# Performance work log

Hardware: AMD Instinct MI355X
Metric: run time of the kernel (lower is better)

## Reference

```python
import jax, jax.numpy as jnp
import numpy as np

B, LT, D, N, H = 16, 512, 1024, 4096, 16
LN_EPS = 1e-5


def setup_inputs() -> dict:
    key = jax.random.key(0)
    ks = jax.random.split(key, 10)
    s = 0.02
    struct_token = jax.random.normal(ks[0], (N, D), dtype=jnp.float32)
    text_token = jax.random.normal(ks[1], (B, LT, D), dtype=jnp.float32)
    # contiguous, sorted segment ids: 256 struct tokens per batch element
    struct_batch = jnp.repeat(jnp.arange(B, dtype=jnp.int32), N // B)
    return {
        "struct_token": struct_token,
        "text_token": text_token,
        "in_proj_w": jax.random.normal(ks[2], (3 * D, D), dtype=jnp.float32) * s,
        "in_proj_b": jnp.zeros((3 * D,), jnp.float32),
        "attn_out_w": jax.random.normal(ks[3], (D, D), dtype=jnp.float32) * s,
        "attn_out_b": jnp.zeros((D,), jnp.float32),
        "ln_g": jnp.ones((D,), jnp.float32),
        "ln_b": jnp.zeros((D,), jnp.float32),
        "proj_w": jax.random.normal(ks[4], (D, D), dtype=jnp.float32) * s,
        "proj_b": jnp.zeros((D,), jnp.float32),
        "struct_batch": struct_batch,
        "L_max": N // B,
    }


def reference(struct_token, text_token, in_proj_w, in_proj_b, attn_out_w,
              attn_out_b, ln_g, ln_b, proj_w, proj_b, struct_batch, L_max):
    Bq = text_token.shape[0]
    Dm = struct_token.shape[-1]
    dh = Dm // H
    Ntok = struct_token.shape[0]

    # ---- ragged pad-pack (struct_batch is sorted/contiguous per segment) ----
    counts = jnp.bincount(struct_batch, length=Bq)                 # [B]
    starts = jnp.concatenate([jnp.zeros((1,), counts.dtype),
                              jnp.cumsum(counts)[:-1]])            # [B]
    pos = jnp.arange(Ntok) - starts[struct_batch]                  # [N] position in segment
    padded = jnp.zeros((Bq, L_max, Dm), struct_token.dtype)
    padded = padded.at[struct_batch, pos].set(struct_token)        # [B, Ls, D]

    # ---- nn.MultiheadAttention (batch_first): Q=padded, K=V=text ----
    wq, wk, wv = in_proj_w[:Dm], in_proj_w[Dm:2 * Dm], in_proj_w[2 * Dm:]
    bq, bk, bv = in_proj_b[:Dm], in_proj_b[Dm:2 * Dm], in_proj_b[2 * Dm:]
    q = (padded @ wq.T + bq).reshape(Bq, L_max, H, dh)
    k = (text_token @ wk.T + bk).reshape(Bq, -1, H, dh)
    v = (text_token @ wv.T + bv).reshape(Bq, -1, H, dh)
    scores = jnp.einsum('bqhd,bkhd->bhqk', q, k) / jnp.sqrt(jnp.float32(dh))
    attn = jax.nn.softmax(scores, axis=-1)
    ctx = jnp.einsum('bhqk,bkhd->bqhd', attn, v).reshape(Bq, L_max, Dm)
    fused = ctx @ attn_out_w.T + attn_out_b                        # [B, Ls, D]

    # ---- LayerNorm + output projection ----
    mu = fused.mean(-1, keepdims=True)
    var = fused.var(-1, keepdims=True)
    fused = (fused - mu) * jax.lax.rsqrt(var + LN_EPS) * ln_g + ln_b
    fused = fused @ proj_w.T + proj_b

    # ---- unpack valid tokens + scatter-mean over segments ----
    tok = fused[struct_batch, pos]                                 # [N, D]
    seg_sum = jax.ops.segment_sum(tok, struct_batch, num_segments=Bq)
    return seg_sum / jnp.maximum(counts, 1)[:, None].astype(seg_sum.dtype)
```

## Files before the change

### kernel.cpp

```cpp
#include <hip/hip_runtime.h>

constexpr int B  = 16;
constexpr int LT = 512;
constexpr int D  = 1024;
constexpr int N  = 4096;
constexpr int H  = 16;
constexpr int DH = D / H;
constexpr int LMAX = N / B;
constexpr float LN_EPS = 1e-5f;

typedef short  s16x8 __attribute__((ext_vector_type(8)));
typedef float  f32x4 __attribute__((ext_vector_type(4)));

__device__ __forceinline__ unsigned short f2bf(float x) {
    unsigned int u = __float_as_uint(x);
    unsigned int r = (u + 0x7fffu + ((u >> 16) & 1u)) >> 16;
    return (unsigned short)r;
}
__device__ __forceinline__ float bf2f(unsigned short u) {
    return __uint_as_float((unsigned int)u << 16);
}

__device__ __forceinline__ void load_lds16(const void* g, void* l) {
    __builtin_amdgcn_global_load_lds(
        (const __attribute__((address_space(1))) unsigned int*)g,
        (__attribute__((address_space(3))) unsigned int*)l, 16, 0, 0);
}

__global__ void prep_kernel(const int* __restrict__ sb, int* __restrict__ counts,
                            int* __restrict__ starts, int* __restrict__ pos) {
    __shared__ int s_counts[B], s_starts[B];
    int t = threadIdx.x;
    if (t < B) s_counts[t] = 0;
    __syncthreads();
    for (int i = t; i < N; i += 256) atomicAdd(&s_counts[sb[i]], 1);
    __syncthreads();
    if (t == 0) {
        int run = 0;
        for (int b = 0; b < B; b++) { s_starts[b] = run; run += s_counts[b]; }
    }
    __syncthreads();
    if (t < B) { counts[t] = s_counts[t]; starts[t] = s_starts[t]; }
    for (int i = t; i < N; i += 256) {
        int b = sb[i];
        pos[i] = i - s_starts[b];
    }
}

__global__ void scatter_kernel(const float* __restrict__ st, const int* __restrict__ sb,
                               const int* __restrict__ pos, unsigned short* __restrict__ padded) {
    int i = blockIdx.x;
    int b = sb[i], p = pos[i];
    int d = threadIdx.x * 4;
    float4 v = *(const float4*)&st[(size_t)i * D + d];
    ushort4 o;
    o.x = f2bf(v.x); o.y = f2bf(v.y); o.z = f2bf(v.z); o.w = f2bf(v.w);
    *(ushort4*)&padded[((size_t)(b * LMAX + p)) * D + d] = o;
}

__global__ __launch_bounds__(256) void cast3_kernel(
        const float* __restrict__ x0, unsigned short* __restrict__ y0, int n0,
        const float* __restrict__ x1, unsigned short* __restrict__ y1, int n1,
        const float* __restrict__ x2, unsigned short* __restrict__ y2, int n2) {
    long long i = (long long)(blockIdx.x * 256 + threadIdx.x) * 8;
    const float* x; unsigned short* y;
    if (i < n0)                { x = x0 + i; y = y0 + i; }
    else if (i < (long long)n0 + n1) { long long j = i - n0; x = x1 + j; y = y1 + j; }
    else if (i < (long long)n0 + n1 + n2) { long long j = i - n0 - n1; x = x2 + j; y = y2 + j; }
    else return;
    float4 a = *(const float4*)x;
    float4 b = *(const float4*)(x + 4);
    ushort4 o1, o2;
    o1.x = f2bf(a.x); o1.y = f2bf(a.y); o1.z = f2bf(a.z); o1.w = f2bf(a.w);
    o2.x = f2bf(b.x); o2.y = f2bf(b.y); o2.z = f2bf(b.z); o2.w = f2bf(b.w);
    *(ushort4*)y = o1;
    *(ushort4*)(y + 4) = o2;
}

constexpr int PANEL = 128 * 32;

template<typename Epi>
__device__ __forceinline__ void gemm_tile_e(const unsigned short* __restrict__ A,
                                            const unsigned short* __restrict__ W,
                                            int K, int m0, int n0,
                                            unsigned short* As, unsigned short* Bs,
                                            Epi&& epi) {
    const int tid  = threadIdx.x;
    const int lane = tid & 63;
    const int wave = tid >> 6;
    const int wm = (wave >> 1) * 64, wn = (wave & 1) * 64;

    const int srow = tid >> 2;
    const int scol = (tid & 3) * 8;
    const unsigned short* Ag = A + (size_t)(m0 + srow) * K + scol;
    const unsigned short* Wg = W + (size_t)(n0 + srow) * K + scol;
    unsigned short* Asl = As + tid * 8;
    unsigned short* Bsl = Bs + tid * 8;

    const int fm = lane & 15;
    const int fk = (lane >> 4) * 8;

    f32x4 acc[4][4];
#pragma unroll
    for (int i = 0; i < 4; i++)
#pragma unroll
        for (int j = 0; j < 4; j++) acc[i][j] = (f32x4){0.f, 0.f, 0.f, 0.f};

    for (int k0 = 0; k0 < K; k0 += 64) {
        __syncthreads();
        load_lds16(Ag + k0, Asl);
        load_lds16(Ag + (size_t)64 * K + k0, Asl + 64 * 32);
        load_lds16(Wg + k0, Bsl);
        load_lds16(Wg + (size_t)64 * K + k0, Bsl + 64 * 32);
        load_lds16(Ag + k0 + 32, Asl + PANEL);
        load_lds16(Ag + (size_t)64 * K + k0 + 32, Asl + PANEL + 64 * 32);
        load_lds16(Wg + k0 + 32, Bsl + PANEL);
        load_lds16(Wg + (size_t)64 * K + k0 + 32, Bsl + PANEL + 64 * 32);
        __syncthreads();

#pragma unroll
        for (int hp = 0; hp < 2; hp++) {
            const unsigned short* Ap = As + hp * PANEL;
            const unsigned short* Bp = Bs + hp * PANEL;
            s16x8 af[4], bf[4];
#pragma unroll
            for (int i = 0; i < 4; i++) {
                af[i] = *(const s16x8*)&Ap[(wm + i * 16 + fm) * 32 + fk];
                bf[i] = *(const s16x8*)&Bp[(wn + i * 16 + fm) * 32 + fk];
            }
#pragma unroll
            for (int i = 0; i < 4; i++)
#pragma unroll
                for (int j = 0; j < 4; j++)
                    acc[i][j] = __builtin_amdgcn_mfma_f32_16x16x32_bf16(af[i], bf[j], acc[i][j], 0, 0, 0);
        }
    }

    const int fr = (lane >> 4) * 4;
#pragma unroll
    for (int j = 0; j < 4; j++) {
        int col = n0 + wn + j * 16 + fm;
#pragma unroll
        for (int i = 0; i < 4; i++) {
            int row = m0 + wm + i * 16 + fr;
#pragma unroll
            for (int r = 0; r < 4; r++)
                epi(row + r, col, acc[i][j][r]);
        }
    }
}

__global__ __launch_bounds__(256) void qkv_fused(const unsigned short* __restrict__ padded,
                                                 const unsigned short* __restrict__ text,
                                                 const unsigned short* __restrict__ wqkv,
                                                 const float* __restrict__ bqkv,
                                                 unsigned short* __restrict__ qpack,
                                                 unsigned short* __restrict__ kpack,
                                                 unsigned short* __restrict__ vpack) {
    __shared__ __align__(16) unsigned short As[2 * PANEL];
    __shared__ __align__(16) unsigned short Bs[2 * PANEL];
    int flat = blockIdx.x;
    if (flat < 256) {
        gemm_tile_e(padded, wqkv, D, (flat >> 3) * 128, (flat & 7) * 128, As, Bs,
            [&](int m, int col, float v) {
                float val = v + bqkv[col];
                int b = m >> 8, q = m & 255;
                int h = col >> 6, d = col & 63;
                qpack[(size_t)(b * H + h) * 16384 + (d >> 3) * 2048 + q * 8 + (d & 7)] = f2bf(val);
            });
    } else if (flat < 768) {
        int f = flat - 256;
        gemm_tile_e(text, wqkv + (size_t)D * D, D, (f >> 3) * 128, (f & 7) * 128, As, Bs,
            [&](int m, int col, float v) {
                float val = v + bqkv[D + col];
                int b = m >> 9, key = m & 511;
                int h = col >> 6, d = col & 63;
                kpack[(size_t)(b * H + h) * 32768 + (d >> 3) * 4096 + key * 8 + (d & 7)] = f2bf(val);
            });
    } else {
        int f = flat - 768;
        gemm_tile_e(wqkv + 2 * (size_t)D * D, text, D, (f >> 6) * 128, (f & 63) * 128, As, Bs,
            [&](int m, int col, float v) {
                float val = v + bqkv[2 * D + m];
                int h = m >> 6, d = m & 63;
                int b = col >> 9, key = col & 511;
                vpack[(size_t)(b * H + h) * 32768 + (key >> 3) * 512 + d * 8 + (key & 7)] = f2bf(val);
            });
    }
}

__global__ __launch_bounds__(256) void gemm_bf(const unsigned short* __restrict__ A,
                                               const unsigned short* __restrict__ W,
                                               const float* __restrict__ bias,
                                               unsigned short* __restrict__ C, int Nn, int K) {
    __shared__ __align__(16) unsigned short As[2 * PANEL];
    __shared__ __align__(16) unsigned short Bs[2 * PANEL];
    gemm_tile_e(A, W, K, blockIdx.y * 128, blockIdx.x * 128, As, Bs,
        [&](int m, int col, float v) {
            C[(size_t)m * Nn + col] = f2bf(v + bias[col]);
        });
}

constexpr int PKW = 72;

__global__ __launch_bounds__(512) void attn_mfma(const unsigned short* __restrict__ qpack,
                                                 const unsigned short* __restrict__ kpack,
                                                 const unsigned short* __restrict__ vpack,
                                                 unsigned short* __restrict__ ctx) {
    __shared__ __align__(16) unsigned short KV[16384];
    __shared__ __align__(16) unsigned short Ps[8 * 16 * PKW];

    const int tid = threadIdx.x;
    const int lane = tid & 63;
    const int wv = tid >> 6;
    const int fm = lane & 15;
    const int quad = lane >> 4;
    const int h = blockIdx.x, b = blockIdx.y, half = blockIdx.z;
    const int q0 = half * 128 + wv * 16;

    const unsigned short* qp = qpack + (size_t)(b * H + h) * 16384;
    const unsigned short* kp = kpack + (size_t)(b * H + h) * 32768;
    const unsigned short* vp = vpack + (size_t)(b * H + h) * 32768;

    const s16x8 aq0 = *(const s16x8*)&qp[quad * 2048 + (q0 + fm) * 8];
    const s16x8 aq1 = *(const s16x8*)&qp[(4 + quad) * 2048 + (q0 + fm) * 8];

    f32x4 sc[32];

    for (int kc = 0; kc < 2; kc++) {
        __syncthreads();
#pragma unroll
        for (int it = 0; it < 4; it++) {
            int f = it * 512 + tid;
            load_lds16(kp + (f >> 8) * 4096 + kc * 2048 + (f & 255) * 8, KV + f * 8);
        }
        __syncthreads();
#pragma unroll
        for (int t = 0; t < 16; t++) {
            s16x8 bk0 = *(const s16x8*)&KV[quad * 2048 + (t * 16 + fm) * 8];
            s16x8 bk1 = *(const s16x8*)&KV[(4 + quad) * 2048 + (t * 16 + fm) * 8];
            f32x4 a = (f32x4){0.f, 0.f, 0.f, 0.f};
            a = __builtin_amdgcn_mfma_f32_16x16x32_bf16(aq0, bk0, a, 0, 0, 0);
            a = __builtin_amdgcn_mfma_f32_16x16x32_bf16(aq1, bk1, a, 0, 0, 0);
            sc[kc * 16 + t] = a;
        }
    }

    const float scale = 0.125f;
    float mx[4], l[4], inv[4];
#pragma unroll
    for (int r = 0; r < 4; r++) {
        float m = sc[0][r];
#pragma unroll
        for (int t = 1; t < 32; t++) m = fmaxf(m, sc[t][r]);
        mx[r] = m;
    }
#pragma unroll
    for (int o = 1; o < 16; o <<= 1)
#pragma unroll
        for (int r = 0; r < 4; r++) mx[r] = fmaxf(mx[r], __shfl_xor(mx[r], o));
#pragma unroll
    for (int r = 0; r < 4; r++) l[r] = 0.f;
#pragma unroll
    for (int t = 0; t < 32; t++)
#pragma unroll
        for (int r = 0; r < 4; r++) {
            float e = __expf((sc[t][r] - mx[r]) * scale);
            sc[t][r] = e;
            l[r] += e;
        }
#pragma unroll
    for (int o = 1; o < 16; o <<= 1)
#pragma unroll
        for (int r = 0; r < 4; r++) l[r] += __shfl_xor(l[r], o);
#pragma unroll
    for (int r = 0; r < 4; r++) inv[r] = 1.f / l[r];

    f32x4 co[4];
#pragma unroll
    for (int n = 0; n < 4; n++) co[n] = (f32x4){0.f, 0.f, 0.f, 0.f};
    unsigned short* Pw = Ps + wv * (16 * PKW);

    for (int vc = 0; vc < 2; vc++) {
        __syncthreads();
#pragma unroll
        for (int it = 0; it < 4; it++) {
            int f = it * 512 + tid;
            load_lds16(vp + vc * 16384 + f * 8, KV + f * 8);
        }
        __syncthreads();
        for (int cs = 0; cs < 4; cs++) {
            int c = vc * 4 + cs;
#pragma unroll
            for (int tt = 0; tt < 4; tt++)
#pragma unroll
                for (int r = 0; r < 4; r++)
                    Pw[(quad * 4 + r) * PKW + tt * 16 + fm] = f2bf(sc[c * 4 + tt][r]);
#pragma unroll
            for (int s = 0; s < 2; s++) {
                s16x8 ap = *(const s16x8*)&Pw[fm * PKW + s * 32 + quad * 8];
#pragma unroll
                for (int n = 0; n < 4; n++) {
                    s16x8 bv = *(const s16x8*)&KV[(cs * 8 + s * 4 + quad) * 512 + (n * 16 + fm) * 8];
                    co[n] = __builtin_amdgcn_mfma_f32_16x16x32_bf16(ap, bv, co[n], 0, 0, 0);
                }
            }
        }
    }

    const size_t obase = (size_t)(b * LMAX + q0) * D + h * DH;
#pragma unroll
    for (int n = 0; n < 4; n++)
#pragma unroll
        for (int r = 0; r < 4; r++)
            ctx[obase + (size_t)(quad * 4 + r) * D + n * 16 + fm] = f2bf(co[n][r] * inv[r]);
}

__global__ __launch_bounds__(256) void lnmean_kernel(const unsigned short* __restrict__ f1,
                                                     const float* __restrict__ g,
                                                     const float* __restrict__ bb,
                                                     const int* __restrict__ counts,
                                                     float* __restrict__ msum) {
    int b = blockIdx.x;
    int cnt = counts[b];
    int s0 = blockIdx.y * 32;
    int s1 = min(cnt, s0 + 32);
    if (s0 >= s1) return;
    int t = threadIdx.x;
    int wv = t >> 6, ln = t & 63;
    float4 gg = ((const float4*)g)[t];
    float4 bv = ((const float4*)bb)[t];
    float acc[4] = {0.f, 0.f, 0.f, 0.f};
    __shared__ float red[8];

    for (int s = s0; s < s1; s++) {
        const unsigned short* x = f1 + ((size_t)(b * LMAX + s)) * D;
        ushort4 u = ((const ushort4*)x)[t];
        float4 val = {bf2f(u.x), bf2f(u.y), bf2f(u.z), bf2f(u.w)};
        float sm = val.x + val.y + val.z + val.w;
        float ss = val.x * val.x + val.y * val.y + val.z * val.z + val.w * val.w;
#pragma unroll
        for (int o = 32; o; o >>= 1) { sm += __shfl_xor(sm, o); ss += __shfl_xor(ss, o); }
        if (ln == 0) { red[wv] = sm; red[4 + wv] = ss; }
        __syncthreads();
        sm = red[0] + red[1] + red[2] + red[3];
        ss = red[4] + red[5] + red[6] + red[7];
        __syncthreads();
        float mu = sm * (1.f / D);
        float var = ss * (1.f / D) - mu * mu;
        float r = rsqrtf(var + LN_EPS);
        acc[0] += (val.x - mu) * r * gg.x + bv.x;
        acc[1] += (val.y - mu) * r * gg.y + bv.y;
        acc[2] += (val.z - mu) * r * gg.z + bv.z;
        acc[3] += (val.w - mu) * r * gg.w + bv.w;
    }
    float inv = 1.f / (float)max(cnt, 1);
#pragma unroll
    for (int j = 0; j < 4; j++)
        atomicAdd(&msum[(size_t)b * D + t * 4 + j], acc[j] * inv);
}

__global__ __launch_bounds__(256) void tproj_kernel(const float* __restrict__ msum,
                                                    const float* __restrict__ W,
                                                    const float* __restrict__ bias,
                                                    float* __restrict__ out) {
    int lane = threadIdx.x & 63;
    int n = blockIdx.x * 4 + (threadIdx.x >> 6);
    float4 wr[4];
#pragma unroll
    for (int i = 0; i < 4; i++)
        wr[i] = *(const float4*)&W[(size_t)n * D + i * 256 + lane * 4];
    float bn = bias[n];
    for (int b = 0; b < B; b++) {
        float s = 0.f;
#pragma unroll
        for (int i = 0; i < 4; i++) {
            float4 m4 = *(const float4*)&msum[(size_t)b * D + i * 256 + lane * 4];
            s += m4.x * wr[i].x + m4.y * wr[i].y + m4.z * wr[i].z + m4.w * wr[i].w;
        }
#pragma unroll
        for (int o = 32; o; o >>= 1) s += __shfl_xor(s, o);
        if (lane == 0) out[(size_t)b * D + n] = s + bn;
    }
}

extern "C" void kernel_launch(void* const* d_in, const int* in_sizes, int n_in,
                              void* d_out, int out_size, void* d_ws, size_t ws_size,
                              hipStream_t stream) {
    const float* struct_token = (const float*)d_in[0];
    const float* text_token   = (const float*)d_in[1];
    const float* in_proj_w    = (const float*)d_in[2];
    const float* in_proj_b    = (const float*)d_in[3];
    const float* attn_out_w   = (const float*)d_in[4];
    const float* attn_out_b   = (const float*)d_in[5];
    const float* ln_g         = (const float*)d_in[6];
    const float* ln_b         = (const float*)d_in[7];
    const float* proj_w       = (const float*)d_in[8];
    const float* proj_b       = (const float*)d_in[9];
    const int*   sb           = (const int*)d_in[10];
    float* out = (float*)d_out;

    const size_t MQ  = (size_t)B * LMAX;
    const size_t MKV = (size_t)B * LT;

    char* p = (char*)d_ws;
    unsigned short* padded_b = (unsigned short*)p;  p += MQ * D * 2;
    unsigned short* text_b   = (unsigned short*)p;  p += MKV * D * 2;
    unsigned short* wqkv_b   = (unsigned short*)p;  p += (size_t)3 * D * D * 2;
    unsigned short* wattn_b  = (unsigned short*)p;  p += (size_t)D * D * 2;
    unsigned short* qpack    = (unsigned short*)p;  p += MQ * D * 2;
    unsigned short* kpack    = (unsigned short*)p;  p += MKV * D * 2;
    unsigned short* vpack    = (unsigned short*)p;  p += MKV * D * 2;
    unsigned short* ctx_b    = (unsigned short*)p;  p += MQ * D * 2;
    unsigned short* f1b      = (unsigned short*)p;  p += MQ * D * 2;
    float* msum = (float*)p;  p += (size_t)B * D * 4;
    int* pos    = (int*)p;  p += N * 4;
    int* counts = (int*)p;  p += B * 4;
    int* starts = (int*)p;  p += B * 4;

    hipMemsetAsync(padded_b, 0, MQ * D * 2, stream);
    hipMemsetAsync(msum, 0, (size_t)B * D * 4, stream);
    prep_kernel<<<1, 256, 0, stream>>>(sb, counts, starts, pos);
    scatter_kernel<<<N, 256, 0, stream>>>(struct_token, sb, pos, padded_b);

    cast3_kernel<<<6144, 256, 0, stream>>>(
        text_token, text_b, (int)(MKV * D),
        in_proj_w,  wqkv_b, 3 * D * D,
        attn_out_w, wattn_b, D * D);

    qkv_fused<<<1280, 256, 0, stream>>>(padded_b, text_b, wqkv_b, in_proj_b,
                                        qpack, kpack, vpack);

    attn_mfma<<<dim3(H, B, 2), 512, 0, stream>>>(qpack, kpack, vpack, ctx_b);

    gemm_bf<<<dim3(D / 128, MQ / 128), 256, 0, stream>>>(ctx_b, wattn_b, attn_out_b, f1b, D, D);

    lnmean_kernel<<<dim3(B, LMAX / 32), 256, 0, stream>>>(f1b, ln_g, ln_b, counts, msum);

    tproj_kernel<<<256, 256, 0, stream>>>(msum, proj_w, proj_b, out);
}
```

Before: 286.7 us.

## Fold segment prep into cast kernel, drop memset and pos, per-wave LayerNorm rows

```diff
diff --git a/kernel.cpp b/kernel.cpp
--- a/kernel.cpp
+++ b/kernel.cpp
@@ -27,42 +27,26 @@
         (__attribute__((address_space(3))) unsigned int*)l, 16, 0, 0);
 }
 
-__global__ void prep_kernel(const int* __restrict__ sb, int* __restrict__ counts,
-                            int* __restrict__ starts, int* __restrict__ pos) {
-    __shared__ int s_counts[B], s_starts[B];
-    int t = threadIdx.x;
-    if (t < B) s_counts[t] = 0;
-    __syncthreads();
-    for (int i = t; i < N; i += 256) atomicAdd(&s_counts[sb[i]], 1);
-    __syncthreads();
-    if (t == 0) {
-        int run = 0;
-        for (int b = 0; b < B; b++) { s_starts[b] = run; run += s_counts[b]; }
-    }
-    __syncthreads();
-    if (t < B) { counts[t] = s_counts[t]; starts[t] = s_starts[t]; }
-    for (int i = t; i < N; i += 256) {
-        int b = sb[i];
-        pos[i] = i - s_starts[b];
-    }
-}
-
-__global__ void scatter_kernel(const float* __restrict__ st, const int* __restrict__ sb,
-                               const int* __restrict__ pos, unsigned short* __restrict__ padded) {
-    int i = blockIdx.x;
-    int b = sb[i], p = pos[i];
-    int d = threadIdx.x * 4;
-    float4 v = *(const float4*)&st[(size_t)i * D + d];
-    ushort4 o;
-    o.x = f2bf(v.x); o.y = f2bf(v.y); o.z = f2bf(v.z); o.w = f2bf(v.w);
-    *(ushort4*)&padded[((size_t)(b * LMAX + p)) * D + d] = o;
-}
-
-__global__ __launch_bounds__(256) void cast3_kernel(
+__global__ __launch_bounds__(256) void cast3_prep(
         const float* __restrict__ x0, unsigned short* __restrict__ y0, int n0,
         const float* __restrict__ x1, unsigned short* __restrict__ y1, int n1,
-        const float* __restrict__ x2, unsigned short* __restrict__ y2, int n2) {
-    long long i = (long long)(blockIdx.x * 256 + threadIdx.x) * 8;
+        const float* __restrict__ x2, unsigned short* __restrict__ y2, int n2,
+        const int* __restrict__ sb, int* __restrict__ counts, int* __restrict__ starts) {
+    __shared__ int s_counts[B];
+    int t = threadIdx.x;
+    if (blockIdx.x == 6144) {
+        if (t < B) s_counts[t] = 0;
+        __syncthreads();
+        for (int i = t; i < N; i += 256) atomicAdd(&s_counts[sb[i]], 1);
+        __syncthreads();
+        if (t == 0) {
+            int run = 0;
+            for (int b = 0; b < B; b++) { starts[b] = run; run += s_counts[b]; }
+        }
+        if (t < B) counts[t] = s_counts[t];
+        return;
+    }
+    long long i = (long long)(blockIdx.x * 256 + t) * 8;
     const float* x; unsigned short* y;
     if (i < n0)                { x = x0 + i; y = y0 + i; }
     else if (i < (long long)n0 + n1) { long long j = i - n0; x = x1 + j; y = y1 + j; }
@@ -75,6 +59,21 @@
     o2.x = f2bf(b.x); o2.y = f2bf(b.y); o2.z = f2bf(b.z); o2.w = f2bf(b.w);
     *(ushort4*)y = o1;
     *(ushort4*)(y + 4) = o2;
+}
+
+__global__ void scatter_full(const float* __restrict__ st,
+                             const int* __restrict__ counts,
+                             const int* __restrict__ starts,
+                             unsigned short* __restrict__ padded) {
+    int p = blockIdx.x, b = blockIdx.y;
+    int d = threadIdx.x * 4;
+    size_t off = ((size_t)(b * LMAX + p)) * D + d;
+    ushort4 o = {0, 0, 0, 0};
+    if (p < counts[b]) {
+        float4 v = *(const float4*)&st[(size_t)(starts[b] + p) * D + d];
+        o.x = f2bf(v.x); o.y = f2bf(v.y); o.z = f2bf(v.z); o.w = f2bf(v.w);
+    }
+    *(ushort4*)&padded[off] = o;
 }
 
 constexpr int PANEL = 128 * 32;
@@ -322,42 +321,55 @@
                                                      const int* __restrict__ counts,
                                                      float* __restrict__ msum) {
     int b = blockIdx.x;
+    int t = threadIdx.x;
+    int wv = t >> 6, lane = t & 63;
     int cnt = counts[b];
-    int s0 = blockIdx.y * 32;
-    int s1 = min(cnt, s0 + 32);
-    if (s0 >= s1) return;
-    int t = threadIdx.x;
-    int wv = t >> 6, ln = t & 63;
-    float4 gg = ((const float4*)g)[t];
-    float4 bv = ((const float4*)bb)[t];
-    float acc[4] = {0.f, 0.f, 0.f, 0.f};
-    __shared__ float red[8];
+    int s0 = blockIdx.y * 32 + wv * 8;
+    int s1 = min(cnt, s0 + 8);
+
+    float4 gg[4], bv[4];
+#pragma unroll
+    for (int c = 0; c < 4; c++) {
+        gg[c] = *(const float4*)&g[c * 256 + lane * 4];
+        bv[c] = *(const float4*)&bb[c * 256 + lane * 4];
+    }
+    float4 acc[4];
+#pragma unroll
+    for (int c = 0; c < 4; c++) acc[c] = (float4){0.f, 0.f, 0.f, 0.f};
 
     for (int s = s0; s < s1; s++) {
         const unsigned short* x = f1 + ((size_t)(b * LMAX + s)) * D;
-        ushort4 u = ((const ushort4*)x)[t];
-        float4 val = {bf2f(u.x), bf2f(u.y), bf2f(u.z), bf2f(u.w)};
-        float sm = val.x + val.y + val.z + val.w;
-        float ss = val.x * val.x + val.y * val.y + val.z * val.z + val.w * val.w;
+        float4 v[4];
+        float sm = 0.f, ss = 0.f;
+#pragma unroll
+        for (int c = 0; c < 4; c++) {
+            ushort4 u = *(const ushort4*)&x[c * 256 + lane * 4];
+            v[c].x = bf2f(u.x); v[c].y = bf2f(u.y); v[c].z = bf2f(u.z); v[c].w = bf2f(u.w);
+            sm += v[c].x + v[c].y + v[c].z + v[c].w;
+            ss += v[c].x * v[c].x + v[c].y * v[c].y + v[c].z * v[c].z + v[c].w * v[c].w;
+        }
 #pragma unroll
         for (int o = 32; o; o >>= 1) { sm += __shfl_xor(sm, o); ss += __shfl_xor(ss, o); }
-        if (ln == 0) { red[wv] = sm; red[4 + wv] = ss; }
-        __syncthreads();
-        sm = red[0] + red[1] + red[2] + red[3];
-        ss = red[4] + red[5] + red[6] + red[7];
-        __syncthreads();
         float mu = sm * (1.f / D);
         float var = ss * (1.f / D) - mu * mu;
         float r = rsqrtf(var + LN_EPS);
-        acc[0] += (val.x - mu) * r * gg.x + bv.x;
-        acc[1] += (val.y - mu) * r * gg.y + bv.y;
-        acc[2] += (val.z - mu) * r * gg.z + bv.z;
-        acc[3] += (val.w - mu) * r * gg.w + bv.w;
+#pragma unroll
+        for (int c = 0; c < 4; c++) {
+            acc[c].x += (v[c].x - mu) * r * gg[c].x + bv[c].x;
+            acc[c].y += (v[c].y - mu) * r * gg[c].y + bv[c].y;
+            acc[c].z += (v[c].z - mu) * r * gg[c].z + bv[c].z;
+            acc[c].w += (v[c].w - mu) * r * gg[c].w + bv[c].w;
+        }
     }
     float inv = 1.f / (float)max(cnt, 1);
 #pragma unroll
-    for (int j = 0; j < 4; j++)
-        atomicAdd(&msum[(size_t)b * D + t * 4 + j], acc[j] * inv);
+    for (int c = 0; c < 4; c++) {
+        int base = b * D + c * 256 + lane * 4;
+        atomicAdd(&msum[base + 0], acc[c].x * inv);
+        atomicAdd(&msum[base + 1], acc[c].y * inv);
+        atomicAdd(&msum[base + 2], acc[c].z * inv);
+        atomicAdd(&msum[base + 3], acc[c].w * inv);
+    }
 }
 
 __global__ __launch_bounds__(256) void tproj_kernel(const float* __restrict__ msum,
@@ -414,19 +426,18 @@
     unsigned short* ctx_b    = (unsigned short*)p;  p += MQ * D * 2;
     unsigned short* f1b      = (unsigned short*)p;  p += MQ * D * 2;
     float* msum = (float*)p;  p += (size_t)B * D * 4;
-    int* pos    = (int*)p;  p += N * 4;
     int* counts = (int*)p;  p += B * 4;
     int* starts = (int*)p;  p += B * 4;
 
-    hipMemsetAsync(padded_b, 0, MQ * D * 2, stream);
     hipMemsetAsync(msum, 0, (size_t)B * D * 4, stream);
-    prep_kernel<<<1, 256, 0, stream>>>(sb, counts, starts, pos);
-    scatter_kernel<<<N, 256, 0, stream>>>(struct_token, sb, pos, padded_b);
-
-    cast3_kernel<<<6144, 256, 0, stream>>>(
+
+    cast3_prep<<<6145, 256, 0, stream>>>(
         text_token, text_b, (int)(MKV * D),
         in_proj_w,  wqkv_b, 3 * D * D,
-        attn_out_w, wattn_b, D * D);
+        attn_out_w, wattn_b, D * D,
+        sb, counts, starts);
+
+    scatter_full<<<dim3(LMAX, B), 256, 0, stream>>>(struct_token, counts, starts, padded_b);
 
     qkv_fused<<<1280, 256, 0, stream>>>(padded_b, text_b, wqkv_b, in_proj_b,
                                         qpack, kpack, vpack);
@@ -435,7 +446,7 @@
 
     gemm_bf<<<dim3(D / 128, MQ / 128), 256, 0, stream>>>(ctx_b, wattn_b, attn_out_b, f1b, D, D);
 
-    lnmean_kernel<<<dim3(B, LMAX / 32), 256, 0, stream>>>(f1b, ln_g, ln_b, counts, msum);
+    lnmean_kernel<<<dim3(B, 8), 256, 0, stream>>>(f1b, ln_g, ln_b, counts, msum);
 
     tproj_kernel<<<256, 256, 0, stream>>>(msum, proj_w, proj_b, out);
 }
```

After: 273.7 us. -4.6%, faster.
